# Kernel optimization log

Hardware: AMD Instinct MI355X
Metric: run time of the kernel (lower is better)

## Reference

```python
import jax, jax.numpy as jnp
import numpy as np
import math

B, LQ, LK, D = 8, 128, 256, 32
ET, H, NH = 32, 8, 64
ETK = ET // H  # 4
LN_EPS = 1e-5


def setup_inputs() -> dict:
    key = jax.random.key(0)
    ks = jax.random.split(key, 12)
    s = 0.02
    return {
        "query_tt": jax.random.uniform(ks[0], (B, LQ), jnp.float32),
        "key_tt": jax.random.uniform(ks[1], (B, LK), jnp.float32),
        "value": jax.random.normal(ks[2], (B, LK, D), jnp.float32),
        "emb_mask": jax.random.randint(ks[3], (B, LK, D), 0, 2, jnp.int32),
        "w_time": jax.random.normal(ks[4], (1, 1), jnp.float32) * s,
        "b_time": jnp.zeros((1,), jnp.float32),
        "w_periodic": jax.random.normal(ks[5], (ET - 1,), jnp.float32) * s,
        "b_periodic": jnp.zeros((ET - 1,), jnp.float32),
        "w_decay": jnp.array([[0.1]], jnp.float32),
        "vt_w1": jax.random.normal(ks[6], (D, NH), jnp.float32) * s,
        "vt_b1": jnp.zeros((NH,), jnp.float32),
        "ln_g": jnp.ones((NH,), jnp.float32),
        "ln_b": jnp.zeros((NH,), jnp.float32),
        "vt_w2": jax.random.normal(ks[7], (NH, D), jnp.float32) * s,
        "vt_b2": jnp.zeros((D,), jnp.float32),
        "wq": jax.random.normal(ks[8], (ET, ET), jnp.float32) * s,
        "bq": jnp.zeros((ET,), jnp.float32),
        "wk": jax.random.normal(ks[9], (ET, ET), jnp.float32) * s,
        "bk": jnp.zeros((ET,), jnp.float32),
        "wo": jax.random.normal(ks[10], (H * D, NH), jnp.float32) * s,
        "bo": jnp.zeros((NH,), jnp.float32),
    }


def _forward(query_tt, key_tt, value, emb_mask, w_time, b_time, w_periodic, b_periodic,
             w_decay, vt_w1, vt_b1, ln_g, ln_b, vt_w2, vt_b2, wq, bq, wk, bk, wo, bo):
    Bv, Lq = query_tt.shape
    Lk = key_tt.shape[1]
    Dv = value.shape[-1]

    # ---- value transfer embedding ----
    v = jnp.broadcast_to(value[:, None, :, :], (Bv, Lq, Lk, Dv))  # [B,Lq,Lk,D]
    d_t = query_tt[:, :, None] - key_tt[:, None, :]               # [B,Lq,Lk]
    hdn = v @ vt_w1 + vt_b1                                       # [B,Lq,Lk,NH]
    mu = hdn.mean(-1, keepdims=True)
    var = ((hdn - mu) ** 2).mean(-1, keepdims=True)
    hdn = (hdn - mu) * jax.lax.rsqrt(var + LN_EPS) * ln_g + ln_b  # LayerNorm
    hdn = jax.nn.relu(hdn)
    d_value = hdn @ vt_w2 + vt_b2                                 # [B,Lq,Lk,D]
    dt1 = d_t[..., None]                                          # [B,Lq,Lk,1]
    time_decay = 1.0 / (1.0 + dt1 * w_decay[0, 0])
    v = d_value * time_decay * dt1 + v                            # [B,Lq,Lk,D]

    # ---- learned time embedding ----
    def time_emb(tt):
        t = tt[..., None]  # [B,L,1]
        return jnp.concatenate([t * w_time[0, 0] + b_time,
                                jnp.sin(t * w_periodic + b_periodic)], axis=-1)  # [B,L,ET]

    q = (time_emb(query_tt) @ wq + bq).reshape(Bv, Lq, H, ETK).transpose(0, 2, 1, 3)  # [B,h,Lq,etk]
    k = (time_emb(key_tt) @ wk + bk).reshape(Bv, Lk, H, ETK).transpose(0, 2, 1, 3)    # [B,h,Lk,etk]

    # ---- per-value-dim attention ----
    scores = jnp.einsum('bhqe,bhke->bhqk', q, k) / math.sqrt(ETK)          # [B,h,Lq,Lk]
    mask5 = emb_mask[:, None, None, :, :]                                   # [B,1,1,Lk,D]
    scores5 = jnp.where(mask5 == 0, jnp.float32(-10000.0), scores[..., None])  # [B,h,Lq,Lk,D]
    p_attn = jax.nn.softmax(scores5, axis=-2)                               # softmax over Lk, per dim d
    x = jnp.einsum('bhqkd,bqkd->bhqd', p_attn, v)                           # [B,h,Lq,D]
    x = x.transpose(0, 2, 1, 3).reshape(Bv, Lq, H * Dv)
    return x @ wo + bo                                                      # [B,Lq,NH]


def reference(query_tt, key_tt, value, emb_mask, w_time, b_time, w_periodic, b_periodic,
              w_decay, vt_w1, vt_b1, ln_g, ln_b, vt_w2, vt_b2, wq, bq, wk, bk, wo, bo):
    return _forward(query_tt, key_tt, value, emb_mask, w_time, b_time, w_periodic, b_periodic,
                    w_decay, vt_w1, vt_b1, ln_g, ln_b, vt_w2, vt_b2, wq, bq, wk, bk, wo, bo)
```

## Files before the change

### kernel.cpp

```cpp
#include <hip/hip_runtime.h>

#define Bv_ 8
#define LQ 128
#define LK 256
#define Dv 32
#define ET 32
#define Hh 8
#define NH 64

typedef __fp16 h2 __attribute__((ext_vector_type(2)));

static __device__ __forceinline__ h2 bch(unsigned u) {
    union { unsigned u; h2 h; } c; c.u = u; return c.h;
}
static __device__ __forceinline__ unsigned pack2(float lo, float hi) {
    union { h2 h; unsigned u; } c;
    c.h = __builtin_amdgcn_cvt_pkrtz(lo, hi);
    return c.u;
}
static __device__ __forceinline__ unsigned short h16(float x) {
    union { __fp16 h; unsigned short u; } c; c.h = (__fp16)x; return c.u;
}
static __device__ __forceinline__ float dot2(h2 a, h2 b, float c) {
#if __has_builtin(__builtin_amdgcn_fdot2)
    return __builtin_amdgcn_fdot2(a, b, c, false);
#else
    return fmaf((float)a.x, (float)b.x, fmaf((float)a.y, (float)b.y, c));
#endif
}

__global__ __launch_bounds__(256) void prep_kernel(
    const float* __restrict__ qtt, const float* __restrict__ ktt,
    const float* __restrict__ value, const int* __restrict__ emb_mask,
    const float* __restrict__ w_time, const float* __restrict__ b_time,
    const float* __restrict__ w_per, const float* __restrict__ b_per,
    const float* __restrict__ vt_w1, const float* __restrict__ vt_b1,
    const float* __restrict__ ln_g, const float* __restrict__ ln_b,
    const float* __restrict__ vt_w2, const float* __restrict__ vt_b2,
    const float* __restrict__ wq, const float* __restrict__ bq,
    const float* __restrict__ wk, const float* __restrict__ bk,
    unsigned* __restrict__ A2g, unsigned* __restrict__ B2g,
    unsigned* __restrict__ M2g,
    float* __restrict__ qe, float* __restrict__ ke)
{
    const int t = threadIdx.x;
    const int blk = blockIdx.x;

    if (blk < 512) {
        __shared__ float vrow[4][Dv];
        __shared__ float hrow[4][NH];
        __shared__ float sha[4][Dv], shb[4][Dv], shm[4][Dv];
        const int w = t >> 6;
        const int l = t & 63;
        const int row = blk * 4 + w;

        if (l < Dv) vrow[w][l] = value[row * Dv + l];
        __syncthreads();

        float h = vt_b1[l];
        #pragma unroll
        for (int d = 0; d < Dv; ++d) h += vrow[w][d] * vt_w1[d * NH + l];

        float s = h;
        #pragma unroll
        for (int off = 32; off > 0; off >>= 1) s += __shfl_xor(s, off);
        const float mu = s * (1.0f / NH);
        const float dc = h - mu;
        float vs = dc * dc;
        #pragma unroll
        for (int off = 32; off > 0; off >>= 1) vs += __shfl_xor(vs, off);
        const float rs = rsqrtf(vs * (1.0f / NH) + 1e-5f);
        hrow[w][l] = fmaxf(dc * rs * ln_g[l] + ln_b[l], 0.0f);
        __syncthreads();

        if (l < Dv) {
            float dval = vt_b2[l];
            #pragma unroll
            for (int j = 0; j < NH; ++j) dval += hrow[w][j] * vt_w2[j * Dv + l];
            const float mm = (emb_mask[row * Dv + l] != 0) ? 1.0f : 0.0f;
            sha[w][l] = mm * vrow[w][l];
            shb[w][l] = mm * dval;
            shm[w][l] = mm;
        }
        __syncthreads();

        if (t < 192) {
            const int arr = t >> 6;
            const int pr  = (t >> 5) & 1;
            const int d   = t & 31;
            float lo, hi;
            unsigned* dst;
            if (arr == 0)      { lo = sha[2*pr][d]; hi = sha[2*pr+1][d]; dst = A2g; }
            else if (arr == 1) { lo = shb[2*pr][d]; hi = shb[2*pr+1][d]; dst = B2g; }
            else               { lo = shm[2*pr][d]; hi = shm[2*pr+1][d]; dst = M2g; }
            dst[(blk * 2 + pr) * 32 + d] = pack2(lo, hi);
        }
    } else {
        const int idx = blk - 512;
        const int sub = t >> 5;
        const int j = t & 31;
        const int row = idx * 8 + sub;
        __shared__ float eb[8][ET];

        float tt;
        const float *W, *bias;
        float* outp;
        if (row < Bv_ * LQ) {
            tt = qtt[row]; W = wq; bias = bq; outp = qe + row * ET;
        } else {
            const int r2 = row - Bv_ * LQ;
            tt = ktt[r2]; W = wk; bias = bk; outp = ke + r2 * ET;
        }
        float e;
        if (j == 0) e = tt * w_time[0] + b_time[0];
        else        e = __sinf(tt * w_per[j - 1] + b_per[j - 1]);
        eb[sub][j] = e;
        __syncthreads();

        float o = bias[j];
        #pragma unroll
        for (int i = 0; i < ET; ++i) o += eb[sub][i] * W[i * ET + j];
        outp[j] = o;
    }
}

__global__ __launch_bounds__(256, 2) void attn_kernel(
    const float* __restrict__ qtt, const float* __restrict__ ktt,
    const float* __restrict__ w_decay,
    const unsigned* __restrict__ A2g, const unsigned* __restrict__ B2g,
    const unsigned* __restrict__ M2g,
    const float* __restrict__ qe, const float* __restrict__ ke,
    const float* __restrict__ wo, const float* __restrict__ bo,
    float* __restrict__ out)
{
    __shared__ __align__(16) unsigned LDSu[17090];
    unsigned* A2s  = LDSu;
    unsigned* B2s  = LDSu + 4096;
    unsigned* M2s  = LDSu + 8192;
    unsigned* E2s  = LDSu + 12288;
    unsigned* EG2s = LDSu + 14400;
    float*    qrs  = (float*)(LDSu + 16512);
    float*    XSH  = (float*)(LDSu + 16576);
    float*    qts  = (float*)(LDSu + 17088);

    const int t = threadIdx.x;
    const int blk = blockIdx.x;
    const int b = blk >> 6;
    const int q0 = (blk & 63) * 2;

    {
        const uint4* Ag = (const uint4*)(A2g + (size_t)b * 4096);
        const uint4* Bg = (const uint4*)(B2g + (size_t)b * 4096);
        const uint4* Mg = (const uint4*)(M2g + (size_t)b * 4096);
        #pragma unroll
        for (int i = 0; i < 4; ++i) {
            const int idx = i * 256 + t;
            ((uint4*)A2s)[idx] = Ag[idx];
            ((uint4*)B2s)[idx] = Bg[idx];
            ((uint4*)M2s)[idx] = Mg[idx];
        }
        if (t < 64) qrs[t] = 0.5f * qe[((size_t)b * LQ + q0) * ET + t];
        if (t < 2)  qts[t] = qtt[b * LQ + q0 + t];
    }
    __syncthreads();

    {
        const int k = t;
        const float4* kerow = (const float4*)(ke + ((size_t)b * LK + k) * ET);
        float4 kr[8];
        #pragma unroll
        for (int h = 0; h < 8; ++h) kr[h] = kerow[h];
        const float ktk = ktt[b * LK + k];
        const float wd = w_decay[0];
        unsigned short* E2u  = (unsigned short*)E2s;
        unsigned short* EG2u = (unsigned short*)EG2s;
        #pragma unroll
        for (int q = 0; q < 2; ++q) {
            const float dt = qts[q] - ktk;
            const float g = dt / fmaf(wd, dt, 1.0f);
            #pragma unroll
            for (int h = 0; h < 8; ++h) {
                const float4 qq = *(const float4*)&qrs[q * 32 + h * 4];
                float sc = qq.x * kr[h].x;
                sc = fmaf(qq.y, kr[h].y, sc);
                sc = fmaf(qq.z, kr[h].z, sc);
                sc = fmaf(qq.w, kr[h].w, sc);
                const float e = __expf(sc);
                E2u[(q * 8 + h) * 264 + k]  = h16(e);
                EG2u[(q * 8 + h) * 264 + k] = h16(e * g);
            }
        }
    }
    __syncthreads();

    const int ks = t >> 5, hg = (t >> 3) & 3, dg = t & 7;
    const int hb = 2 * hg;
    float accN[2][2][4] = {{{0}}}, accD[2][2][4] = {{{0}}};
    {
        const unsigned* Eb  = E2s  + ks * 16;
        const unsigned* EGb = EG2s + ks * 16;
        const unsigned* Ab = A2s + ks * 512 + dg * 4;
        const unsigned* Bb = B2s + ks * 512 + dg * 4;
        const unsigned* Mb = M2s + ks * 512 + dg * 4;
        #pragma unroll
        for (int si = 0; si < 4; ++si) {
            unsigned eu[2][2][4], egu[2][2][4];
            unsigned au[4][4], bu[4][4], mu_[4][4];
            #pragma unroll
            for (int q = 0; q < 2; ++q) {
                #pragma unroll
                for (int hh = 0; hh < 2; ++hh) {
                    const uint4 v = *(const uint4*)(Eb  + (q*8 + hb + hh)*132 + si*4);
                    const uint4 w = *(const uint4*)(EGb + (q*8 + hb + hh)*132 + si*4);
                    eu[q][hh][0]=v.x; eu[q][hh][1]=v.y; eu[q][hh][2]=v.z; eu[q][hh][3]=v.w;
                    egu[q][hh][0]=w.x; egu[q][hh][1]=w.y; egu[q][hh][2]=w.z; egu[q][hh][3]=w.w;
                }
            }
            #pragma unroll
            for (int j = 0; j < 4; ++j) {
                const uint4 a  = *(const uint4*)(Ab + (si*4 + j)*32);
                const uint4 bb = *(const uint4*)(Bb + (si*4 + j)*32);
                const uint4 m  = *(const uint4*)(Mb + (si*4 + j)*32);
                au[j][0]=a.x; au[j][1]=a.y; au[j][2]=a.z; au[j][3]=a.w;
                bu[j][0]=bb.x; bu[j][1]=bb.y; bu[j][2]=bb.z; bu[j][3]=bb.w;
                mu_[j][0]=m.x; mu_[j][1]=m.y; mu_[j][2]=m.z; mu_[j][3]=m.w;
            }
            #pragma unroll
            for (int q = 0; q < 2; ++q)
            #pragma unroll
            for (int hh = 0; hh < 2; ++hh)
            #pragma unroll
            for (int j = 0; j < 4; ++j) {
                const h2 e2  = bch(eu[q][hh][j]);
                const h2 eg2 = bch(egu[q][hh][j]);
                #pragma unroll
                for (int dd = 0; dd < 4; ++dd) {
                    accN[q][hh][dd] = dot2(e2,  bch(au[j][dd]),  accN[q][hh][dd]);
                    accN[q][hh][dd] = dot2(eg2, bch(bu[j][dd]),  accN[q][hh][dd]);
                    accD[q][hh][dd] = dot2(e2,  bch(mu_[j][dd]), accD[q][hh][dd]);
                }
            }
        }
    }
    __syncthreads();

    float* REDN = (float*)A2s;
    float* REDD = (float*)B2s;
    #pragma unroll
    for (int q = 0; q < 2; ++q)
    #pragma unroll
    for (int hh = 0; hh < 2; ++hh) {
        const int c = (q * 8 + hb + hh) * 32 + dg * 4;
        *(float4*)&REDN[ks * 512 + c] =
            make_float4(accN[q][hh][0], accN[q][hh][1], accN[q][hh][2], accN[q][hh][3]);
        *(float4*)&REDD[ks * 512 + c] =
            make_float4(accD[q][hh][0], accD[q][hh][1], accD[q][hh][2], accD[q][hh][3]);
    }
    __syncthreads();

    if (t < 128) {
        float4 n = make_float4(0.f,0.f,0.f,0.f), d = make_float4(0.f,0.f,0.f,0.f);
        #pragma unroll
        for (int s = 0; s < 8; ++s) {
            const float4 nn = *(const float4*)&REDN[s * 512 + t * 4];
            const float4 dd = *(const float4*)&REDD[s * 512 + t * 4];
            n.x += nn.x; n.y += nn.y; n.z += nn.z; n.w += nn.w;
            d.x += dd.x; d.y += dd.y; d.z += dd.z; d.w += dd.w;
        }
        float4 x;
        x.x = n.x / fmaxf(d.x, 1e-30f);
        x.y = n.y / fmaxf(d.y, 1e-30f);
        x.z = n.z / fmaxf(d.z, 1e-30f);
        x.w = n.w / fmaxf(d.w, 1e-30f);
        *(float4*)&XSH[t * 4] = x;
    }
    __syncthreads();

    if (t < 128) {
        const int q = t >> 6, j = t & 63;
        float acc = bo[j];
        const float4* xq = (const float4*)&XSH[q * 256];
        #pragma unroll 8
        for (int c4 = 0; c4 < 64; ++c4) {
            const float4 xv = xq[c4];
            const int c = c4 * 4;
            acc = fmaf(xv.x, wo[(c + 0) * NH + j], acc);
            acc = fmaf(xv.y, wo[(c + 1) * NH + j], acc);
            acc = fmaf(xv.z, wo[(c + 2) * NH + j], acc);
            acc = fmaf(xv.w, wo[(c + 3) * NH + j], acc);
        }
        out[((size_t)b * LQ + q0 + q) * NH + j] = acc;
    }
}

extern "C" void kernel_launch(void* const* d_in, const int* in_sizes, int n_in,
                              void* d_out, int out_size, void* d_ws, size_t ws_size,
                              hipStream_t stream) {
    const float* qtt      = (const float*)d_in[0];
    const float* ktt      = (const float*)d_in[1];
    const float* value    = (const float*)d_in[2];
    const int*   emb_mask = (const int*)  d_in[3];
    const float* w_time   = (const float*)d_in[4];
    const float* b_time   = (const float*)d_in[5];
    const float* w_per    = (const float*)d_in[6];
    const float* b_per    = (const float*)d_in[7];
    const float* w_decay  = (const float*)d_in[8];
    const float* vt_w1    = (const float*)d_in[9];
    const float* vt_b1    = (const float*)d_in[10];
    const float* ln_g     = (const float*)d_in[11];
    const float* ln_b     = (const float*)d_in[12];
    const float* vt_w2    = (const float*)d_in[13];
    const float* vt_b2    = (const float*)d_in[14];
    const float* wq       = (const float*)d_in[15];
    const float* bq       = (const float*)d_in[16];
    const float* wk       = (const float*)d_in[17];
    const float* bk       = (const float*)d_in[18];
    const float* wo       = (const float*)d_in[19];
    const float* bo       = (const float*)d_in[20];
    float* out = (float*)d_out;

    unsigned* wsu = (unsigned*)d_ws;
    unsigned* A2g = wsu;
    unsigned* B2g = wsu + 32768;
    unsigned* M2g = wsu + 65536;
    float*    qew = (float*)(wsu + 98304);
    float*    kew = (float*)(wsu + 131072);

    hipLaunchKernelGGL(prep_kernel, dim3(896), dim3(256), 0, stream,
                       qtt, ktt, value, emb_mask, w_time, b_time, w_per, b_per,
                       vt_w1, vt_b1, ln_g, ln_b, vt_w2, vt_b2,
                       wq, bq, wk, bk, A2g, B2g, M2g, qew, kew);

    hipLaunchKernelGGL(attn_kernel, dim3(512), dim3(256), 0, stream,
                       qtt, ktt, w_decay, A2g, B2g, M2g, qew, kew, wo, bo, out);
}
```

Baseline: 110.7 us.

## Stage global loads in registers, store only decay factor in LDS, parallelize output projection

Global loads of the A/B/M tables and the key embeddings are issued into registers up front, so the score/exp computation overlaps their latency and one barrier is removed. The per-(q,h) e*g array is replaced by a per-q decay array g; e*g is formed on the fly with a packed half multiply, which cuts LDS writes and reads and shrinks shared memory. The output projection now uses all 256 threads with float4 weight loads and a shuffle reduction instead of 128 threads doing serial scalar loads. The cost is more live registers and an extra fp16 multiply that adds rounding.

```diff
diff --git a/kernel.cpp b/kernel.cpp
--- a/kernel.cpp
+++ b/kernel.cpp
@@ -133,21 +133,24 @@
     const float* __restrict__ wo, const float* __restrict__ bo,
     float* __restrict__ out)
 {
-    __shared__ __align__(16) unsigned LDSu[17090];
-    unsigned* A2s  = LDSu;
-    unsigned* B2s  = LDSu + 4096;
-    unsigned* M2s  = LDSu + 8192;
-    unsigned* E2s  = LDSu + 12288;
-    unsigned* EG2s = LDSu + 14400;
-    float*    qrs  = (float*)(LDSu + 16512);
-    float*    XSH  = (float*)(LDSu + 16576);
-    float*    qts  = (float*)(LDSu + 17088);
+    __shared__ __align__(16) unsigned LDSu[14664];
+    unsigned* A2s = LDSu;
+    unsigned* B2s = LDSu + 4096;
+    unsigned* M2s = LDSu + 8192;
+    unsigned* E2s = LDSu + 12288;
+    unsigned* G2s = LDSu + 14400;
 
     const int t = threadIdx.x;
     const int blk = blockIdx.x;
     const int b = blk >> 6;
     const int q0 = (blk & 63) * 2;
 
+    const float4* kerow = (const float4*)(ke + ((size_t)b * LK + t) * ET);
+    float4 kr[8];
+    #pragma unroll
+    for (int h = 0; h < 8; ++h) kr[h] = kerow[h];
+
+    uint4 pa[4], pb[4], pm[4];
     {
         const uint4* Ag = (const uint4*)(A2g + (size_t)b * 4096);
         const uint4* Bg = (const uint4*)(B2g + (size_t)b * 4096);
@@ -155,41 +158,42 @@
         #pragma unroll
         for (int i = 0; i < 4; ++i) {
             const int idx = i * 256 + t;
-            ((uint4*)A2s)[idx] = Ag[idx];
-            ((uint4*)B2s)[idx] = Bg[idx];
-            ((uint4*)M2s)[idx] = Mg[idx];
-        }
-        if (t < 64) qrs[t] = 0.5f * qe[((size_t)b * LQ + q0) * ET + t];
-        if (t < 2)  qts[t] = qtt[b * LQ + q0 + t];
-    }
-    __syncthreads();
+            pa[i] = Ag[idx]; pb[i] = Bg[idx]; pm[i] = Mg[idx];
+        }
+    }
 
     {
-        const int k = t;
-        const float4* kerow = (const float4*)(ke + ((size_t)b * LK + k) * ET);
-        float4 kr[8];
-        #pragma unroll
-        for (int h = 0; h < 8; ++h) kr[h] = kerow[h];
-        const float ktk = ktt[b * LK + k];
+        const float ktk = ktt[b * LK + t];
         const float wd = w_decay[0];
-        unsigned short* E2u  = (unsigned short*)E2s;
-        unsigned short* EG2u = (unsigned short*)EG2s;
+        unsigned short* E2u = (unsigned short*)E2s;
+        unsigned short* G2u = (unsigned short*)G2s;
+        #pragma unroll
+        for (int h = 0; h < 8; ++h) {
+            kr[h].x *= 0.5f; kr[h].y *= 0.5f; kr[h].z *= 0.5f; kr[h].w *= 0.5f;
+        }
         #pragma unroll
         for (int q = 0; q < 2; ++q) {
-            const float dt = qts[q] - ktk;
-            const float g = dt / fmaf(wd, dt, 1.0f);
+            const float dt = qtt[b * LQ + q0 + q] - ktk;
+            G2u[q * 264 + t] = h16(dt / fmaf(wd, dt, 1.0f));
+            const float4* qrow = (const float4*)(qe + ((size_t)b * LQ + q0 + q) * ET);
             #pragma unroll
             for (int h = 0; h < 8; ++h) {
-                const float4 qq = *(const float4*)&qrs[q * 32 + h * 4];
+                const float4 qq = qrow[h];
                 float sc = qq.x * kr[h].x;
                 sc = fmaf(qq.y, kr[h].y, sc);
                 sc = fmaf(qq.z, kr[h].z, sc);
                 sc = fmaf(qq.w, kr[h].w, sc);
-                const float e = __expf(sc);
-                E2u[(q * 8 + h) * 264 + k]  = h16(e);
-                EG2u[(q * 8 + h) * 264 + k] = h16(e * g);
+                E2u[(q * 8 + h) * 264 + t] = h16(__expf(sc));
             }
         }
+    }
+
+    #pragma unroll
+    for (int i = 0; i < 4; ++i) {
+        const int idx = i * 256 + t;
+        ((uint4*)A2s)[idx] = pa[i];
+        ((uint4*)B2s)[idx] = pb[i];
+        ((uint4*)M2s)[idx] = pm[i];
     }
     __syncthreads();
 
@@ -197,24 +201,24 @@
     const int hb = 2 * hg;
     float accN[2][2][4] = {{{0}}}, accD[2][2][4] = {{{0}}};
     {
-        const unsigned* Eb  = E2s  + ks * 16;
-        const unsigned* EGb = EG2s + ks * 16;
+        const unsigned* Eb = E2s + ks * 16;
+        const unsigned* Gb = G2s + ks * 16;
         const unsigned* Ab = A2s + ks * 512 + dg * 4;
         const unsigned* Bb = B2s + ks * 512 + dg * 4;
         const unsigned* Mb = M2s + ks * 512 + dg * 4;
         #pragma unroll
         for (int si = 0; si < 4; ++si) {
-            unsigned eu[2][2][4], egu[2][2][4];
+            unsigned eu[2][2][4];
+            uint4 gu[2];
             unsigned au[4][4], bu[4][4], mu_[4][4];
             #pragma unroll
             for (int q = 0; q < 2; ++q) {
                 #pragma unroll
                 for (int hh = 0; hh < 2; ++hh) {
-                    const uint4 v = *(const uint4*)(Eb  + (q*8 + hb + hh)*132 + si*4);
-                    const uint4 w = *(const uint4*)(EGb + (q*8 + hb + hh)*132 + si*4);
+                    const uint4 v = *(const uint4*)(Eb + (q*8 + hb + hh)*132 + si*4);
                     eu[q][hh][0]=v.x; eu[q][hh][1]=v.y; eu[q][hh][2]=v.z; eu[q][hh][3]=v.w;
-                    egu[q][hh][0]=w.x; egu[q][hh][1]=w.y; egu[q][hh][2]=w.z; egu[q][hh][3]=w.w;
                 }
+                gu[q] = *(const uint4*)(Gb + q*132 + si*4);
             }
             #pragma unroll
             for (int j = 0; j < 4; ++j) {
@@ -226,18 +230,20 @@
                 mu_[j][0]=m.x; mu_[j][1]=m.y; mu_[j][2]=m.z; mu_[j][3]=m.w;
             }
             #pragma unroll
-            for (int q = 0; q < 2; ++q)
-            #pragma unroll
-            for (int hh = 0; hh < 2; ++hh)
-            #pragma unroll
-            for (int j = 0; j < 4; ++j) {
-                const h2 e2  = bch(eu[q][hh][j]);
-                const h2 eg2 = bch(egu[q][hh][j]);
+            for (int q = 0; q < 2; ++q) {
+                const unsigned gq[4] = {gu[q].x, gu[q].y, gu[q].z, gu[q].w};
                 #pragma unroll
-                for (int dd = 0; dd < 4; ++dd) {
-                    accN[q][hh][dd] = dot2(e2,  bch(au[j][dd]),  accN[q][hh][dd]);
-                    accN[q][hh][dd] = dot2(eg2, bch(bu[j][dd]),  accN[q][hh][dd]);
-                    accD[q][hh][dd] = dot2(e2,  bch(mu_[j][dd]), accD[q][hh][dd]);
+                for (int hh = 0; hh < 2; ++hh)
+                #pragma unroll
+                for (int j = 0; j < 4; ++j) {
+                    const h2 e2  = bch(eu[q][hh][j]);
+                    const h2 eg2 = e2 * bch(gq[j]);
+                    #pragma unroll
+                    for (int dd = 0; dd < 4; ++dd) {
+                        accN[q][hh][dd] = dot2(e2,  bch(au[j][dd]),  accN[q][hh][dd]);
+                        accN[q][hh][dd] = dot2(eg2, bch(bu[j][dd]),  accN[q][hh][dd]);
+                        accD[q][hh][dd] = dot2(e2,  bch(mu_[j][dd]), accD[q][hh][dd]);
+                    }
                 }
             }
         }
@@ -246,6 +252,7 @@
 
     float* REDN = (float*)A2s;
     float* REDD = (float*)B2s;
+    float* XSH  = (float*)M2s;
     #pragma unroll
     for (int q = 0; q < 2; ++q)
     #pragma unroll
@@ -276,20 +283,36 @@
     }
     __syncthreads();
 
-    if (t < 128) {
-        const int q = t >> 6, j = t & 63;
-        float acc = bo[j];
-        const float4* xq = (const float4*)&XSH[q * 256];
+    {
+        const int q  = t >> 7;
+        const int j4 = (t >> 3) & 15;
+        const int cs = t & 7;
+        const float* xq = XSH + q * 256;
+        float4 a4 = make_float4(0.f, 0.f, 0.f, 0.f);
         #pragma unroll 8
-        for (int c4 = 0; c4 < 64; ++c4) {
-            const float4 xv = xq[c4];
-            const int c = c4 * 4;
-            acc = fmaf(xv.x, wo[(c + 0) * NH + j], acc);
-            acc = fmaf(xv.y, wo[(c + 1) * NH + j], acc);
-            acc = fmaf(xv.z, wo[(c + 2) * NH + j], acc);
-            acc = fmaf(xv.w, wo[(c + 3) * NH + j], acc);
-        }
-        out[((size_t)b * LQ + q0 + q) * NH + j] = acc;
+        for (int cc = 0; cc < 32; ++cc) {
+            const int c = cs * 32 + ((cc + 4 * cs) & 31);
+            const float xv = xq[c];
+            const float4 wv = *(const float4*)&wo[c * NH + j4 * 4];
+            a4.x = fmaf(xv, wv.x, a4.x);
+            a4.y = fmaf(xv, wv.y, a4.y);
+            a4.z = fmaf(xv, wv.z, a4.z);
+            a4.w = fmaf(xv, wv.w, a4.w);
+        }
+        #pragma unroll
+        for (int off = 1; off < 8; off <<= 1) {
+            a4.x += __shfl_xor(a4.x, off);
+            a4.y += __shfl_xor(a4.y, off);
+            a4.z += __shfl_xor(a4.z, off);
+            a4.w += __shfl_xor(a4.w, off);
+        }
+        if (cs == 0) {
+            const float4 bv = *(const float4*)&bo[j4 * 4];
+            float4 o;
+            o.x = a4.x + bv.x; o.y = a4.y + bv.y;
+            o.z = a4.z + bv.z; o.w = a4.w + bv.w;
+            *(float4*)&out[((size_t)b * LQ + q0 + q) * NH + j4 * 4] = o;
+        }
     }
 }
 
```

Result: slower. 113.2 us (+2.3%).
